# Performance work log

Measured on AMD Instinct MI355X. Metric: run time of the kernel, lower is better.

## Reference

```python
import jax, jax.numpy as jnp
import numpy as np

H, P, G, N, K, CS = 64, 64, 8, 128, 4, 256
HID = 2048
INTER = H * P                      # 4096
CONV_D = INTER + 2 * G * N         # 6144
PROJ = INTER + CONV_D + H          # 10304
EPS = 1e-5


def setup_inputs() -> dict:
    key = jax.random.key(0)
    ks = jax.random.split(key, 4)
    B_, L_ = 2, 2048
    return {
        "hidden_states": jax.random.normal(ks[0], (B_, L_, HID), jnp.float32),
        "in_proj_w": jax.random.normal(ks[1], (PROJ, HID), jnp.float32) * 0.02,
        "conv_w": jax.random.normal(ks[2], (CONV_D, K), jnp.float32) * 0.2,
        "conv_b": jnp.zeros((CONV_D,), jnp.float32),
        "dt_bias": jnp.ones((H,), jnp.float32),
        "A_log": jnp.log(jnp.arange(1, H + 1, dtype=jnp.float32)),
        "D": jnp.ones((H,), jnp.float32),
        "norm_w": jnp.ones((INTER,), jnp.float32),
        "out_proj_w": jax.random.normal(ks[3], (HID, INTER), jnp.float32) * 0.02,
    }


def reference(hidden_states, in_proj_w, conv_w, conv_b, dt_bias, A_log, D, norm_w, out_proj_w):
    b, l, _ = hidden_states.shape
    r = H // G  # heads per group

    zxbcdt = hidden_states @ in_proj_w.T                      # [b,l,PROJ]
    z = zxbcdt[..., :INTER]
    xBC = zxbcdt[..., INTER:INTER + CONV_D]
    dt = zxbcdt[..., INTER + CONV_D:]                          # [b,l,H]

    # causal depthwise conv1d (kernel K, left pad K-1) + SiLU
    xp = jnp.pad(xBC, ((0, 0), (K - 1, 0), (0, 0)))
    conv = conv_b
    for i in range(K):
        conv = conv + conv_w[:, i] * xp[:, i:i + l, :]
    xBC = jax.nn.silu(conv)

    x = xBC[..., :INTER]
    Bm = xBC[..., INTER:INTER + G * N]
    Cm = xBC[..., INTER + G * N:]

    dt = jax.nn.softplus(dt + dt_bias)                         # [b,l,H]
    A = -jnp.exp(A_log)                                        # [H]

    nc = l // CS
    x_c = x.reshape(b, nc, CS, G, r, P)
    dt_c = dt.reshape(b, nc, CS, G, r)
    B_c = Bm.reshape(b, nc, CS, G, N)
    C_c = Cm.reshape(b, nc, CS, G, N)

    dA = dt_c * A.reshape(G, r)                                # [b,nc,c,g,r]
    dA_cs = jnp.cumsum(dA, axis=2)                             # inclusive cumsum over chunk

    # intra-chunk: L[i,j] = exp(dA_cs[i]-dA_cs[j]) for i>=j
    diff = dA_cs[:, :, :, None] - dA_cs[:, :, None]            # [b,nc,i,j,g,r]
    mask = jnp.tril(jnp.ones((CS, CS), bool))[None, None, :, :, None, None]
    Lmat = jnp.exp(jnp.where(mask, diff, -jnp.inf))
    CB = jnp.einsum('bzign,bzjgn->bzijg', C_c, B_c)            # per-group C·B
    M = CB[..., None] * Lmat * dt_c[:, :, None]                # [b,nc,i,j,g,r]
    Y_diag = jnp.einsum('bzijgr,bzjgrp->bzigrp', M, x_c)

    # per-chunk end states
    w = jnp.exp(dA_cs[:, :, -1:] - dA_cs) * dt_c               # decay to chunk end * dt
    states = jnp.einsum('bzjgn,bzjgr,bzjgrp->bzgrpn', B_c, w, x_c)  # [b,nc,g,r,p,n]
    chunk_decay = jnp.exp(dA_cs[:, :, -1])                     # [b,nc,g,r]

    def step(S, inp):
        d, s = inp
        return d[..., None, None] * S + s, S                   # emit state BEFORE chunk

    init = jnp.zeros((b, G, r, P, N), x.dtype)
    _, prev = jax.lax.scan(step, init, (jnp.moveaxis(chunk_decay, 1, 0), jnp.moveaxis(states, 1, 0)))
    prev = jnp.moveaxis(prev, 0, 1)                            # [b,nc,g,r,p,n]

    Y_off = jnp.einsum('bzign,bzgrpn->bzigrp', C_c, prev) * jnp.exp(dA_cs)[..., None]

    Y = (Y_diag + Y_off).reshape(b, l, H, P) + D[:, None] * x.reshape(b, l, H, P)
    y = Y.reshape(b, l, INTER)

    # gated RMSNorm, norm_before_gate=True: out = rmsnorm(y) * silu(z)
    var = jnp.mean(y * y, axis=-1, keepdims=True)
    y = norm_w * (y * jax.lax.rsqrt(var + EPS)) * jax.nn.silu(z)

    return y @ out_proj_w.T
```

## Files before the change

kernel.cpp:

```cpp
#include <hip/hip_runtime.h>
#include <hip/hip_bf16.h>
#include <cstdint>
#include <cstddef>

#define H_     64
#define P_     64
#define G_     8
#define N_     128
#define K_     4
#define CS_    256
#define HID_   2048
#define INTER_ 4096
#define CONVD_ 6144
#define PROJ_  10304
#define ZSTR_  10240
#define B_     2
#define L_     2048
#define NC_    8
#define ML_    4096
#define EPS_   1e-5f

typedef unsigned short ushort_t;
typedef __attribute__((ext_vector_type(8))) short short8;
typedef __attribute__((ext_vector_type(4))) float f32x4;

__device__ inline float b2f(ushort_t v) {
  unsigned u = ((unsigned)v) << 16;
  float f;
  __builtin_memcpy(&f, &u, 4);
  return f;
}
__device__ inline ushort_t f2b(float f) {
  unsigned u;
  __builtin_memcpy(&u, &f, 4);
  u = u + 0x7FFFu + ((u >> 16) & 1u);
  return (ushort_t)(u >> 16);
}
__device__ inline void ld_bf8(const ushort_t* p, float* f) {
  uint4 u = *(const uint4*)p;
  const ushort_t* s = (const ushort_t*)&u;
#pragma unroll
  for (int c = 0; c < 8; ++c) f[c] = b2f(s[c]);
}
__device__ inline void st_bf8(ushort_t* p, const float* f) {
  uint4 u;
  ushort_t* s = (ushort_t*)&u;
#pragma unroll
  for (int c = 0; c < 8; ++c) s[c] = f2b(f[c]);
  *(uint4*)p = u;
}

__global__ __launch_bounds__(256) void cast1_k(const float* __restrict__ hs,
                                               const float* __restrict__ w_in,
                                               ushort_t* __restrict__ hsb,
                                               ushort_t* __restrict__ w_inb) {
  size_t e8 = ((size_t)blockIdx.x * 256 + threadIdx.x) * 8;
  const float* src;
  ushort_t* dst;
  const size_t HSN = (size_t)ML_ * HID_;
  if (e8 < HSN) { src = hs + e8; dst = hsb + e8; }
  else          { src = w_in + (e8 - HSN); dst = w_inb + (e8 - HSN); }
  float4 a = *(const float4*)src;
  float4 b = *(const float4*)(src + 4);
  float v[8] = {a.x, a.y, a.z, a.w, b.x, b.y, b.z, b.w};
  st_bf8(dst, v);
}

typedef const __attribute__((address_space(1))) unsigned int gu32;
typedef __attribute__((address_space(3))) unsigned int lu32;
__device__ __forceinline__ void gl_lds16(const ushort_t* g, ushort_t* l) {
  __builtin_amdgcn_global_load_lds((gu32*)g, (lu32*)l, 16, 0, 0);
}

template<int N> __device__ __forceinline__ void wait_vmcnt() {
  if constexpr (N == 8)      asm volatile("s_waitcnt vmcnt(8)" ::: "memory");
  else if constexpr (N == 6) asm volatile("s_waitcnt vmcnt(6)" ::: "memory");
  else if constexpr (N == 4) asm volatile("s_waitcnt vmcnt(4)" ::: "memory");
  else if constexpr (N == 3) asm volatile("s_waitcnt vmcnt(3)" ::: "memory");
  else                       asm volatile("s_waitcnt vmcnt(0)" ::: "memory");
}

template<int MR>
__device__ __forceinline__ void gemm_core(const ushort_t* __restrict__ Ag,
                                          const ushort_t* __restrict__ Bg,
                                          int lda, int ldb, int nkt,
                                          int bm, int bn, int brmax,
                                          ushort_t* __restrict__ As,
                                          ushort_t* __restrict__ Bs,
                                          f32x4 (&acc)[MR / 32][4]) {
  constexpr int MF = MR / 32;
  constexpr int ASLOT = MR * 32;
  constexpr int BSLOT = 256 * 32;
  constexpr int LPT = (MR == 256) ? 4 : 3;
  const int t = threadIdx.x;
  const int w = t >> 6, l = t & 63;
  const int wm = w >> 2, wn = w & 3;
  const int ml = l & 15, q = l >> 4;
  const int swz = (ml >> 1) & 3;
  const int aoff = (wm * (MR / 2) + ml) * 32 + ((q ^ swz) << 3);
  const int boff = (wn * 64 + ml) * 32 + ((q ^ swz) << 3);
  const int permc = (((l & 3) ^ ((l >> 3) & 3)) << 3);
  const ushort_t* ag0 = Ag + (size_t)(bm + (MR / 8) * w + (l >> 2)) * lda + permc;
  const ushort_t* ag1 = ag0 + (size_t)16 * lda;
  int br0 = bn + 32 * w + (l >> 2);      if (br0 > brmax) br0 = brmax;
  int br1 = bn + 32 * w + 16 + (l >> 2); if (br1 > brmax) br1 = brmax;
  const ushort_t* bg0 = Bg + (size_t)br0 * ldb + permc;
  const ushort_t* bg1 = Bg + (size_t)br1 * ldb + permc;
  ushort_t* alw = As + ((MR == 256) ? (2 * w * 512) : (w * 512));
  ushort_t* blw = Bs + 2 * w * 512;

#define STAGE_A_(kt_)                                                        \
  { const int k_ = (kt_) << 5;                                               \
    ushort_t* sa_ = alw + ((kt_) & 3) * ASLOT;                               \
    gl_lds16(ag0 + k_, sa_);                                                 \
    if (MR == 256) gl_lds16(ag1 + k_, sa_ + 512); }
#define STAGE_B_(kt_)                                                        \
  { const int k_ = (kt_) << 5;                                               \
    ushort_t* sb_ = blw + ((kt_) & 3) * BSLOT;                               \
    gl_lds16(bg0 + k_, sb_);                                                 \
    gl_lds16(bg1 + k_, sb_ + 512); }

  STAGE_A_(0); STAGE_B_(0);
  STAGE_A_(1); STAGE_B_(1);
  STAGE_A_(2); STAGE_B_(2);

#pragma unroll
  for (int i = 0; i < MF; ++i)
#pragma unroll
    for (int j = 0; j < 4; ++j) acc[i][j] = (f32x4){0.f, 0.f, 0.f, 0.f};

#pragma unroll 1
  for (int kt = 0; kt < nkt; ++kt) {
    const ushort_t* Asl = As + (kt & 3) * ASLOT;
    const ushort_t* Bsl = Bs + (kt & 3) * BSLOT;
    if (kt + 2 < nkt)      wait_vmcnt<2 * LPT>();
    else if (kt + 1 < nkt) wait_vmcnt<LPT>();
    else                   wait_vmcnt<0>();
    __builtin_amdgcn_s_barrier();
    asm volatile("" ::: "memory");
    const bool st = (kt + 3) < nkt;
    short8 bfr[4], af[MF / 2];
#pragma unroll
    for (int nf = 0; nf < 4; ++nf)
      bfr[nf] = *(const short8*)(Bsl + boff + nf * 512);
#pragma unroll
    for (int mf = 0; mf < MF / 2; ++mf)
      af[mf] = *(const short8*)(Asl + aoff + mf * 512);
    if (st) STAGE_A_(kt + 3);
    __builtin_amdgcn_s_setprio(1);
#pragma unroll
    for (int mf = 0; mf < MF / 2; ++mf)
#pragma unroll
      for (int nf = 0; nf < 4; ++nf)
        acc[mf][nf] = __builtin_amdgcn_mfma_f32_16x16x32_bf16(af[mf], bfr[nf], acc[mf][nf], 0, 0, 0);
    __builtin_amdgcn_s_setprio(0);
#pragma unroll
    for (int mf = 0; mf < MF / 2; ++mf)
      af[mf] = *(const short8*)(Asl + aoff + (mf + MF / 2) * 512);
    if (st) STAGE_B_(kt + 3);
    __builtin_amdgcn_s_setprio(1);
#pragma unroll
    for (int mf = 0; mf < MF / 2; ++mf)
#pragma unroll
      for (int nf = 0; nf < 4; ++nf)
        acc[mf + MF / 2][nf] = __builtin_amdgcn_mfma_f32_16x16x32_bf16(af[mf], bfr[nf], acc[mf + MF / 2][nf], 0, 0, 0);
    __builtin_amdgcn_s_setprio(0);
  }
#undef STAGE_A_
#undef STAGE_B_
}

__global__ __launch_bounds__(512, 2) void gemm1_256(const ushort_t* __restrict__ hsb,
                                                    const ushort_t* __restrict__ w_inb,
                                                    ushort_t* __restrict__ zb,
                                                    float* __restrict__ dtraw) {
  __shared__ __align__(16) ushort_t As[4 * 8192];
  __shared__ __align__(16) ushort_t Bs[4 * 8192];
  int bid = blockIdx.x;
  int wg = (bid & 7) * 82 + (bid >> 3);
  int tm = wg & 15, tn = wg >> 4;
  int bm = tm * 256, bn = tn * 256;
  f32x4 acc[8][4];
  gemm_core<256>(hsb, w_inb, HID_, HID_, HID_ / 32, bm, bn, PROJ_ - 1, As, Bs, acc);
  int t = threadIdx.x, w = t >> 6, l = t & 63;
  int wm = w >> 2, wn = w & 3, ml = l & 15, quad = l >> 4;
  int rb = bm + wm * 128 + quad * 4;
  int cb = bn + wn * 64 + ml;
  if (tn < 40) {
#pragma unroll
    for (int mf = 0; mf < 8; ++mf)
#pragma unroll
      for (int r = 0; r < 4; ++r) {
        size_t row = (size_t)(rb + mf * 16 + r) * ZSTR_;
#pragma unroll
        for (int nf = 0; nf < 4; ++nf)
          zb[row + cb + nf * 16] = f2b(acc[mf][nf][r]);
      }
  } else if (wn == 0) {
#pragma unroll
    for (int mf = 0; mf < 8; ++mf)
#pragma unroll
      for (int r = 0; r < 4; ++r) {
        int tok = rb + mf * 16 + r;
#pragma unroll
        for (int nf = 0; nf < 4; ++nf)
          dtraw[(size_t)(ml + nf * 16) * ML_ + tok] = acc[mf][nf][r];
      }
  }
}

__global__ __launch_bounds__(512, 2) void gemm2_128(const ushort_t* __restrict__ Ab,
                                                    const ushort_t* __restrict__ Bb,
                                                    float* __restrict__ C) {
  __shared__ __align__(16) ushort_t As[4 * 4096];
  __shared__ __align__(16) ushort_t Bs[4 * 8192];
  int bid = blockIdx.x;
  int wg = (bid & 7) * 32 + (bid >> 3);
  int tm = wg & 31, tn = wg >> 5;
  int bm = tm * 128, bn = tn * 256;
  f32x4 acc[4][4];
  gemm_core<128>(Ab, Bb, CONVD_, INTER_, INTER_ / 32, bm, bn, HID_ - 1, As, Bs, acc);
  int t = threadIdx.x, w = t >> 6, l = t & 63;
  int wm = w >> 2, wn = w & 3, ml = l & 15, quad = l >> 4;
  int rb = bm + wm * 64 + quad * 4;
  int cb = bn + wn * 64 + ml;
#pragma unroll
  for (int mf = 0; mf < 4; ++mf)
#pragma unroll
    for (int r = 0; r < 4; ++r) {
      size_t row = (size_t)(rb + mf * 16 + r) * HID_;
#pragma unroll
      for (int nf = 0; nf < 4; ++nf)
        C[row + cb + nf * 16] = acc[mf][nf][r];
    }
}

#define CROWS_ 8
__global__ __launch_bounds__(256) void conv_dt_k(const ushort_t* __restrict__ zb,
                                                 const float* __restrict__ cw,
                                                 const float* __restrict__ cb,
                                                 ushort_t* __restrict__ xcb,
                                                 const float* __restrict__ dtraw,
                                                 const float* __restrict__ dt_bias,
                                                 const float* __restrict__ A_log,
                                                 float* __restrict__ dtp,
                                                 float* __restrict__ dacs,
                                                 float* __restrict__ cdec) {
  __shared__ float sm[256];
  int bid = blockIdx.x;
  if (bid < 1536) {
    int grp = bid & 511;
    int seg = bid >> 9;
    int u = threadIdx.x;
    int c8 = seg * 2048 + u * 8;
    int row0 = grp * CROWS_;
    int l0 = row0 & (L_ - 1);

    float wv[K_][8], bias[8];
    {
      const float4* wp = (const float4*)(cw + (size_t)c8 * K_);
#pragma unroll
      for (int c = 0; c < 8; ++c) {
        float4 w4 = wp[c];
        wv[0][c] = w4.x; wv[1][c] = w4.y; wv[2][c] = w4.z; wv[3][c] = w4.w;
      }
      float4 b0 = *(const float4*)(cb + c8);
      float4 b1 = *(const float4*)(cb + c8 + 4);
      bias[0] = b0.x; bias[1] = b0.y; bias[2] = b0.z; bias[3] = b0.w;
      bias[4] = b1.x; bias[5] = b1.y; bias[6] = b1.z; bias[7] = b1.w;
    }
    const ushort_t* xin = zb + (size_t)row0 * ZSTR_ + INTER_ + c8;
    ushort_t* xout = xcb + (size_t)row0 * CONVD_ + c8;

    float win[4][8];
#pragma unroll
    for (int i = 0; i < 3; ++i) {
      if (l0 > 0) {
        ld_bf8(xin + (ptrdiff_t)(i - 3) * ZSTR_, win[i]);
      } else {
#pragma unroll
        for (int c = 0; c < 8; ++c) win[i][c] = 0.f;
      }
    }
#pragma unroll
    for (int r = 0; r < CROWS_; ++r) {
      ld_bf8(xin + (size_t)r * ZSTR_, win[(r + 3) & 3]);
      float a[8];
#pragma unroll
      for (int c = 0; c < 8; ++c) {
        float v = bias[c];
        v = fmaf(wv[0][c], win[(r + 0) & 3][c], v);
        v = fmaf(wv[1][c], win[(r + 1) & 3][c], v);
        v = fmaf(wv[2][c], win[(r + 2) & 3][c], v);
        v = fmaf(wv[3][c], win[(r + 3) & 3][c], v);
        a[c] = v / (1.f + __expf(-v));
      }
      st_bf8(xout + (size_t)r * CONVD_, a);
    }
  } else {
    int bzh = bid - 1536;
    int h = bzh & 63, z = (bzh >> 6) & 7, b = bzh >> 9;
    int i = threadIdx.x;
    size_t row = (size_t)b * L_ + z * CS_ + i;
    float dv = dtraw[(size_t)h * ML_ + row] + dt_bias[h];
    float sp = (dv > 20.f) ? dv : log1pf(expf(dv));
    float v = sp * (-expf(A_log[h]));
    sm[i] = v;
    __syncthreads();
    for (int off = 1; off < 256; off <<= 1) {
      float add = (i >= off) ? sm[i - off] : 0.f;
      __syncthreads();
      sm[i] += add;
      __syncthreads();
    }
    float cs = sm[i];
    size_t ob = ((size_t)b * H_ + h) * L_ + z * CS_ + i;
    dtp[ob] = sp;
    dacs[ob] = cs;
    if (i == CS_ - 1) cdec[bzh] = expf(cs);
  }
}

__global__ __launch_bounds__(256) void cb_k(const ushort_t* __restrict__ xcb,
                                            ushort_t* __restrict__ CBo) {
  static const unsigned char itab[10] = {0, 1, 1, 2, 2, 2, 3, 3, 3, 3};
  static const unsigned char jtab[10] = {0, 0, 1, 0, 1, 2, 0, 1, 2, 3};
  int tp = blockIdx.x;
  int it = itab[tp], jt = jtab[tp];
  int bzg = blockIdx.y;
  int g = bzg & 7, z = (bzg >> 3) & 7, b = bzg >> 6;
  int t = threadIdx.x;
  int tx = t & 15, ty = t >> 4;
  __shared__ float CtT[64][68];
  __shared__ float BtT[64][68];
  size_t rowbase = (size_t)b * L_ + (size_t)z * CS_;
  float acc[4][4];
#pragma unroll
  for (int i = 0; i < 4; ++i)
#pragma unroll
    for (int j = 0; j < 4; ++j) acc[i][j] = 0.f;

  for (int half = 0; half < 2; ++half) {
    int nb = half * 64;
    __syncthreads();
#pragma unroll
    for (int u = 0; u < 2; ++u) {
      int idx = t + u * 256;
      int rr = idx >> 3, f = idx & 7;
      float cv[8], bv[8];
      ld_bf8(xcb + (rowbase + it * 64 + rr) * CONVD_ + INTER_ + G_ * N_ + g * N_ + nb + f * 8, cv);
      ld_bf8(xcb + (rowbase + jt * 64 + rr) * CONVD_ + INTER_ + g * N_ + nb + f * 8, bv);
#pragma unroll
      for (int c = 0; c < 8; ++c) { CtT[f * 8 + c][rr] = cv[c]; BtT[f * 8 + c][rr] = bv[c]; }
    }
    __syncthreads();
    for (int n = 0; n < 64; ++n) {
      float4 cv = *(const float4*)&CtT[n][ty * 4];
      float4 bv = *(const float4*)&BtT[n][tx * 4];
      float cc[4] = {cv.x, cv.y, cv.z, cv.w};
      float bb[4] = {bv.x, bv.y, bv.z, bv.w};
#pragma unroll
      for (int i = 0; i < 4; ++i)
#pragma unroll
        for (int j = 0; j < 4; ++j) acc[i][j] = fmaf(cc[i], bb[j], acc[i][j]);
    }
  }
  size_t cbase = ((size_t)((b * 8 + z) * 8 + g)) * (CS_ * CS_);
#pragma unroll
  for (int i = 0; i < 4; ++i) {
    int row = it * 64 + ty * 4 + i;
    ushort4 v;
    v.x = f2b(acc[i][0]); v.y = f2b(acc[i][1]); v.z = f2b(acc[i][2]); v.w = f2b(acc[i][3]);
    *(ushort4*)(CBo + cbase + (size_t)row * CS_ + jt * 64 + tx * 4) = v;
  }
}

__global__ __launch_bounds__(256) void states_mfma(const ushort_t* __restrict__ xcb,
                                                   const float* __restrict__ dacs,
                                                   const float* __restrict__ dtp,
                                                   float* __restrict__ st) {
  int bzh = blockIdx.x;
  int h = bzh & 63, z = (bzh >> 6) & 7, b = bzh >> 9;
  int g = h >> 3;
  int t = threadIdx.x;
  int wv = t >> 6, lane = t & 63;
  int ml = lane & 15, ko = (lane >> 4) * 8;
  __shared__ float ws[256];
  __shared__ __align__(16) ushort_t Xw[64 * 136];
  __shared__ __align__(16) ushort_t Bt[128 * 136];
  size_t base = ((size_t)b * H_ + h) * L_ + z * CS_;
  float dlast = dacs[base + CS_ - 1];
  ws[t] = __expf(dlast - dacs[base + t]) * dtp[base + t];
  size_t rowbase = (size_t)b * L_ + z * CS_;
  f32x4 acc[4][2];
#pragma unroll
  for (int i = 0; i < 4; ++i) {
    acc[i][0] = (f32x4){0.f, 0.f, 0.f, 0.f};
    acc[i][1] = (f32x4){0.f, 0.f, 0.f, 0.f};
  }
  for (int half = 0; half < 2; ++half) {
    int j0 = half * 128;
    __syncthreads();
    {
      int jl = t >> 1, pseg = (t & 1) * 32;
      const ushort_t* xr = xcb + (rowbase + j0 + jl) * CONVD_ + h * P_ + pseg;
      float wj = ws[j0 + jl];
#pragma unroll
      for (int q = 0; q < 4; ++q) {
        float v[8];
        ld_bf8(xr + q * 8, v);
#pragma unroll
        for (int c = 0; c < 8; ++c) Xw[(pseg + q * 8 + c) * 136 + jl] = f2b(v[c] * wj);
      }
    }
    {
      int jl = t >> 1, nseg = (t & 1) * 64;
      const ushort_t* br = xcb + (rowbase + j0 + jl) * CONVD_ + INTER_ + g * N_ + nseg;
#pragma unroll
      for (int q = 0; q < 8; ++q) {
        uint4 raw = *(const uint4*)(br + q * 8);
        const ushort_t* s = (const ushort_t*)&raw;
#pragma unroll
        for (int c = 0; c < 8; ++c) Bt[(nseg + q * 8 + c) * 136 + jl] = s[c];
      }
    }
    __syncthreads();
#pragma unroll
    for (int k0 = 0; k0 < 128; k0 += 32) {
      short8 af[4], bf2[2];
#pragma unroll
      for (int mf = 0; mf < 4; ++mf)
        af[mf] = *(const short8*)(Xw + (mf * 16 + ml) * 136 + k0 + ko);
#pragma unroll
      for (int nf = 0; nf < 2; ++nf)
        bf2[nf] = *(const short8*)(Bt + (wv * 32 + nf * 16 + ml) * 136 + k0 + ko);
#pragma unroll
      for (int mf = 0; mf < 4; ++mf)
#pragma unroll
        for (int nf = 0; nf < 2; ++nf)
          acc[mf][nf] = __builtin_amdgcn_mfma_f32_16x16x32_bf16(af[mf], bf2[nf], acc[mf][nf], 0, 0, 0);
    }
  }
  float* outp = st + ((size_t)((b * 8 + z) * H_ + h)) * (P_ * N_);
  int quad = lane >> 4;
#pragma unroll
  for (int mf = 0; mf < 4; ++mf)
#pragma unroll
    for (int nf = 0; nf < 2; ++nf) {
      int n = wv * 32 + nf * 16 + ml;
#pragma unroll
      for (int r = 0; r < 4; ++r) {
        int p = mf * 16 + quad * 4 + r;
        outp[(size_t)p * N_ + n] = acc[mf][nf][r];
      }
    }
}

__global__ __launch_bounds__(256) void scan_k(float* __restrict__ st,
                                              const float* __restrict__ cdec) {
  size_t idx = (size_t)blockIdx.x * 256 + threadIdx.x;
  int b = (int)(idx >> 19);
  size_t rem = idx & 524287;
  int h = (int)(rem >> 13);
  float S = 0.f;
#pragma unroll
  for (int z = 0; z < NC_; ++z) {
    size_t off = (size_t)(b * 8 + z) * 524288 + rem;
    float old = st[off];
    st[off] = S;
    S = cdec[(b * 8 + z) * H_ + h] * S + old;
  }
}

__global__ __launch_bounds__(256) void y_mfma(const ushort_t* xcb,
                                              const ushort_t* __restrict__ CB,
                                              const float* __restrict__ pv,
                                              const float* __restrict__ dacs,
                                              const float* __restrict__ dtp,
                                              const float* __restrict__ Dw,
                                              ushort_t* Yx) {
  int bzh = blockIdx.x;
  int h = bzh & 63, z = (bzh >> 6) & 7, b = bzh >> 9;
  int g = h >> 3;
  int t = threadIdx.x;
  int wv = t >> 6, lane = t & 63;
  int ml = lane & 15, quad = lane >> 4, ko = quad * 8;
  __shared__ __align__(16) ushort_t Ms[256 * 40];
  __shared__ __align__(16) ushort_t XsYs[18432];
  __shared__ __align__(16) ushort_t Ps[64 * 136];
  __shared__ float dAs[256], dts[256];

  size_t rowbase = (size_t)b * L_ + z * CS_;
  {
    size_t base = ((size_t)b * H_ + h) * L_ + z * CS_;
    dAs[t] = dacs[base + t];
    dts[t] = dtp[base + t];
  }
  {
    int p = t >> 2, c0 = (t & 3) * 32;
    const float* pr = pv + ((size_t)((b * 8 + z) * H_ + h)) * (P_ * N_) + (size_t)p * N_ + c0;
    ushort_t* dst = Ps + p * 136 + c0;
#pragma unroll
    for (int u = 0; u < 4; ++u) {
      float4 a = *(const float4*)(pr + u * 8);
      float4 bq = *(const float4*)(pr + u * 8 + 4);
      float v[8] = {a.x, a.y, a.z, a.w, bq.x, bq.y, bq.z, bq.w};
      st_bf8(dst + u * 8, v);
    }
  }
  {
    const ushort_t* xr = xcb + (rowbase + t) * CONVD_ + h * P_;
    ushort_t* Xs = XsYs;
#pragma unroll
    for (int q = 0; q < 8; ++q) {
      uint4 raw = *(const uint4*)(xr + q * 8);
      const ushort_t* s = (const ushort_t*)&raw;
#pragma unroll
      for (int c = 0; c < 8; ++c) Xs[(q * 8 + c) * 264 + t] = s[c];
    }
  }

  f32x4 acc[4][4];
#pragma unroll
  for (int i = 0; i < 4; ++i)
#pragma unroll
    for (int j = 0; j < 4; ++j) acc[i][j] = (f32x4){0.f, 0.f, 0.f, 0.f};

  int cOff = INTER_ + G_ * N_ + g * N_;
#pragma unroll
  for (int k0 = 0; k0 < 128; k0 += 32) {
    __syncthreads();
#pragma unroll
    for (int u = 0; u < 4; ++u) {
      int sid = u * 256 + t;
      int row = sid >> 2, kc = (sid & 3) * 8;
      gl_lds16(xcb + (rowbase + row) * CONVD_ + cOff + k0 + kc,
               Ms + (size_t)(u * 256 + wv * 64) * 8);
    }
    __syncthreads();
    short8 af[4], bf[4];
#pragma unroll
    for (int mf = 0; mf < 4; ++mf)
      af[mf] = *(const short8*)(Ps + (mf * 16 + ml) * 136 + k0 + ko);
#pragma unroll
    for (int nf = 0; nf < 4; ++nf)
      bf[nf] = *(const short8*)(Ms + (wv * 64 + nf * 16 + ml) * 32 + ko);
#pragma unroll
    for (int mf = 0; mf < 4; ++mf)
#pragma unroll
      for (int nf = 0; nf < 4; ++nf)
        acc[mf][nf] = __builtin_amdgcn_mfma_f32_16x16x32_bf16(af[mf], bf[nf], acc[mf][nf], 0, 0, 0);
  }
#pragma unroll
  for (int nf = 0; nf < 4; ++nf) {
    float e = __expf(dAs[wv * 64 + nf * 16 + ml]);
#pragma unroll
    for (int mf = 0; mf < 4; ++mf) {
      acc[mf][nf][0] *= e; acc[mf][nf][1] *= e;
      acc[mf][nf][2] *= e; acc[mf][nf][3] *= e;
    }
  }

  float dAi_t = dAs[t];
  size_t cbase = ((size_t)((b * 8 + z) * 8 + g)) * (CS_ * CS_) + (size_t)t * CS_;
  const ushort_t* Xs = XsYs;
  for (int j0 = 0; j0 < 256; j0 += 32) {
    __syncthreads();
    {
      const ushort_t* cbr = CB + cbase + j0;
      ushort_t* mrow = Ms + t * 40;
#pragma unroll
      for (int q = 0; q < 4; ++q) {
        float cv[8], o[8];
        ld_bf8(cbr + q * 8, cv);
#pragma unroll
        for (int c = 0; c < 8; ++c) {
          int j = j0 + q * 8 + c;
          float m = cv[c] * __expf(dAi_t - dAs[j]) * dts[j];
          o[c] = (j <= t) ? m : 0.f;
        }
        st_bf8(mrow + q * 8, o);
      }
    }
    __syncthreads();
    short8 af[4], bf[4];
#pragma unroll
    for (int mf = 0; mf < 4; ++mf)
      af[mf] = *(const short8*)(Xs + (mf * 16 + ml) * 264 + j0 + ko);
#pragma unroll
    for (int nf = 0; nf < 4; ++nf)
      bf[nf] = *(const short8*)(Ms + (wv * 64 + nf * 16 + ml) * 40 + ko);
#pragma unroll
    for (int mf = 0; mf < 4; ++mf)
#pragma unroll
      for (int nf = 0; nf < 4; ++nf)
        acc[mf][nf] = __builtin_amdgcn_mfma_f32_16x16x32_bf16(af[mf], bf[nf], acc[mf][nf], 0, 0, 0);
  }

  __syncthreads();
  ushort_t* Ys = XsYs;
#pragma unroll
  for (int mf = 0; mf < 4; ++mf)
#pragma unroll
    for (int nf = 0; nf < 4; ++nf) {
      int iw = wv * 64 + nf * 16 + ml;
      int pb = mf * 16 + quad * 4;
      uint2 pk;
      ushort_t* s = (ushort_t*)&pk;
      s[0] = f2b(acc[mf][nf][0]); s[1] = f2b(acc[mf][nf][1]);
      s[2] = f2b(acc[mf][nf][2]); s[3] = f2b(acc[mf][nf][3]);
      *(uint2*)(Ys + iw * 72 + pb) = pk;
    }
  __syncthreads();
  {
    float Dh = Dw[h];
    const ushort_t* xr = xcb + (rowbase + t) * CONVD_ + h * P_;
    ushort_t* yr = Yx + (rowbase + t) * CONVD_ + h * P_;
#pragma unroll
    for (int q = 0; q < 8; ++q) {
      float xv[8], yv[8], o[8];
      ld_bf8(xr + q * 8, xv);
      ld_bf8(Ys + t * 72 + q * 8, yv);
#pragma unroll
      for (int c = 0; c < 8; ++c) o[c] = yv[c] + Dh * xv[c];
      st_bf8(yr + q * 8, o);
    }
  }
}

__global__ __launch_bounds__(256) void rms_cast2_k(ushort_t* __restrict__ Y,
                                                   const ushort_t* __restrict__ zb,
                                                   const float* __restrict__ nw,
                                                   const float* __restrict__ w_out,
                                                   ushort_t* __restrict__ w_outb) {
  __shared__ float red[4];
  int bid = blockIdx.x;
  int t = threadIdx.x;
  if (bid >= ML_) {
    size_t e8 = ((size_t)(bid - ML_) * 256 + t) * 8;
    float4 a = *(const float4*)(w_out + e8);
    float4 b = *(const float4*)(w_out + e8 + 4);
    float v[8] = {a.x, a.y, a.z, a.w, b.x, b.y, b.z, b.w};
    st_bf8(w_outb + e8, v);
    return;
  }
  int row = bid;
  ushort_t* y = Y + (size_t)row * CONVD_;
  const ushort_t* zp = zb + (size_t)row * ZSTR_;
  float v[2][8];
  float s = 0.f;
#pragma unroll
  for (int u = 0; u < 2; ++u) {
    ld_bf8(y + u * 2048 + t * 8, v[u]);
#pragma unroll
    for (int c = 0; c < 8; ++c) s += v[u][c] * v[u][c];
  }
#pragma unroll
  for (int off = 32; off > 0; off >>= 1) s += __shfl_down(s, off);
  if ((t & 63) == 0) red[t >> 6] = s;
  __syncthreads();
  float tot = red[0] + red[1] + red[2] + red[3];
  float rstd = rsqrtf(tot * (1.f / INTER_) + EPS_);
#pragma unroll
  for (int u = 0; u < 2; ++u) {
    int c0 = u * 2048 + t * 8;
    float zv[8], o[8];
    ld_bf8(zp + c0, zv);
    float4 w0 = *(const float4*)(nw + c0);
    float4 w1 = *(const float4*)(nw + c0 + 4);
    float wv[8] = {w0.x, w0.y, w0.z, w0.w, w1.x, w1.y, w1.z, w1.w};
#pragma unroll
    for (int c = 0; c < 8; ++c)
      o[c] = wv[c] * v[u][c] * rstd * (zv[c] / (1.f + __expf(-zv[c])));
    st_bf8(y + c0, o);
  }
}

extern "C" void kernel_launch(void* const* d_in, const int* in_sizes, int n_in,
                              void* d_out, int out_size, void* d_ws, size_t ws_size,
                              hipStream_t stream) {
  const float* hs    = (const float*)d_in[0];
  const float* w_in  = (const float*)d_in[1];
  const float* cw    = (const float*)d_in[2];
  const float* cb    = (const float*)d_in[3];
  const float* dtb   = (const float*)d_in[4];
  const float* alog  = (const float*)d_in[5];
  const float* Dw    = (const float*)d_in[6];
  const float* nw    = (const float*)d_in[7];
  const float* w_out = (const float*)d_in[8];
  float* out = (float*)d_out;

  char* base = (char*)d_ws;
  ushort_t* zb    = (ushort_t*)(base);
  ushort_t* xcb   = (ushort_t*)(base + 83886080);
  float*    dtraw = (float*)(base + 134217728);
  float*    dtp   = (float*)(base + 135266304);
  float*    dacs  = (float*)(base + 136314880);
  float*    cdec  = (float*)(base + 137363456);
  char*     R1    = base + 137367552;
  char*     R2    = base + 154144768;
  ushort_t* hsb    = (ushort_t*)R1;
  ushort_t* cbuf   = (ushort_t*)R1;
  ushort_t* w_outb = (ushort_t*)R1;
  ushort_t* w_inb  = (ushort_t*)R2;
  float*    st     = (float*)R2;

  cast1_k<<<14400, 256, 0, stream>>>(hs, w_in, hsb, w_inb);
  gemm1_256<<<656, 512, 0, stream>>>(hsb, w_inb, zb, dtraw);
  conv_dt_k<<<2560, 256, 0, stream>>>(zb, cw, cb, xcb, dtraw, dtb, alog, dtp, dacs, cdec);
  cb_k<<<dim3(10, B_ * NC_ * G_), 256, 0, stream>>>(xcb, cbuf);
  states_mfma<<<B_ * NC_ * H_, 256, 0, stream>>>(xcb, dacs, dtp, st);
  scan_k<<<(B_ * H_ * P_ * N_) / 256, 256, 0, stream>>>(st, cdec);
  y_mfma<<<B_ * NC_ * H_, 256, 0, stream>>>(xcb, cbuf, st, dacs, dtp, Dw, xcb);
  rms_cast2_k<<<8192, 256, 0, stream>>>(xcb, zb, nw, w_out, w_outb);
  gemm2_128<<<256, 512, 0, stream>>>(xcb, w_outb, out);
}
```

Measured before the change: 629.6 us.

## Use MFMA for C·B chunk products, pack LDS transposes, prefetch CB tiles

The cb_k kernel now stages C and B tiles into LDS as bf16 with direct global-to-LDS loads and an XOR swizzle. It then computes the 64x64 block with bf16 MFMA instructions in place of scalar fp32 FMAs. In states_mfma, the transposed X and B tiles are written as packed 32-bit pairs of adjacent rows, which halves the number of LDS stores. In the diagonal output kernel, the next 32-column slice of the CB matrix is register-prefetched during the MFMA loop to hide global load latency. The final per-element scalar bf16 stores in cb_k may be less coalesced than the previous 4-wide stores.

```diff
diff --git a/kernel.cpp b/kernel.cpp
--- a/kernel.cpp
+++ b/kernel.cpp
@@ -330,49 +330,63 @@
   int bzg = blockIdx.y;
   int g = bzg & 7, z = (bzg >> 3) & 7, b = bzg >> 6;
   int t = threadIdx.x;
-  int tx = t & 15, ty = t >> 4;
-  __shared__ float CtT[64][68];
-  __shared__ float BtT[64][68];
+  int w = t >> 6, l = t & 63;
+  __shared__ __align__(16) ushort_t Cs[64 * 128];
+  __shared__ __align__(16) ushort_t Bs[64 * 128];
   size_t rowbase = (size_t)b * L_ + (size_t)z * CS_;
-  float acc[4][4];
-#pragma unroll
-  for (int i = 0; i < 4; ++i)
-#pragma unroll
-    for (int j = 0; j < 4; ++j) acc[i][j] = 0.f;
-
-  for (int half = 0; half < 2; ++half) {
-    int nb = half * 64;
-    __syncthreads();
-#pragma unroll
-    for (int u = 0; u < 2; ++u) {
-      int idx = t + u * 256;
-      int rr = idx >> 3, f = idx & 7;
-      float cv[8], bv[8];
-      ld_bf8(xcb + (rowbase + it * 64 + rr) * CONVD_ + INTER_ + G_ * N_ + g * N_ + nb + f * 8, cv);
-      ld_bf8(xcb + (rowbase + jt * 64 + rr) * CONVD_ + INTER_ + g * N_ + nb + f * 8, bv);
-#pragma unroll
-      for (int c = 0; c < 8; ++c) { CtT[f * 8 + c][rr] = cv[c]; BtT[f * 8 + c][rr] = bv[c]; }
-    }
-    __syncthreads();
-    for (int n = 0; n < 64; ++n) {
-      float4 cv = *(const float4*)&CtT[n][ty * 4];
-      float4 bv = *(const float4*)&BtT[n][tx * 4];
-      float cc[4] = {cv.x, cv.y, cv.z, cv.w};
-      float bb[4] = {bv.x, bv.y, bv.z, bv.w};
-#pragma unroll
-      for (int i = 0; i < 4; ++i)
-#pragma unroll
-        for (int j = 0; j < 4; ++j) acc[i][j] = fmaf(cc[i], bb[j], acc[i][j]);
-    }
+  {
+    int s = l & 15;
+    int cO = INTER_ + G_ * N_ + g * N_;
+    int bO = INTER_ + g * N_;
+#pragma unroll
+    for (int i = 0; i < 4; ++i) {
+      int row = 16 * w + 4 * i + (l >> 4);
+      int src = ((s ^ (row & 15)) << 3);
+      gl_lds16(xcb + (rowbase + it * 64 + row) * CONVD_ + cO + src,
+               Cs + (16 * w + 4 * i) * 128);
+      gl_lds16(xcb + (rowbase + jt * 64 + row) * CONVD_ + bO + src,
+               Bs + (16 * w + 4 * i) * 128);
+    }
+  }
+  asm volatile("s_waitcnt vmcnt(0)" ::: "memory");
+  __builtin_amdgcn_s_barrier();
+  int wm = w >> 1, wn = w & 1;
+  int ml = l & 15, q = l >> 4;
+  f32x4 acc[2][2];
+#pragma unroll
+  for (int i = 0; i < 2; ++i)
+#pragma unroll
+    for (int j = 0; j < 2; ++j) acc[i][j] = (f32x4){0.f, 0.f, 0.f, 0.f};
+#pragma unroll
+  for (int kk = 0; kk < 4; ++kk) {
+    short8 af[2], bf[2];
+#pragma unroll
+    for (int mf = 0; mf < 2; ++mf) {
+      int row = wm * 32 + mf * 16 + ml;
+      af[mf] = *(const short8*)(Cs + row * 128 + (((kk * 4 + q) ^ (row & 15)) << 3));
+    }
+#pragma unroll
+    for (int nf = 0; nf < 2; ++nf) {
+      int row = wn * 32 + nf * 16 + ml;
+      bf[nf] = *(const short8*)(Bs + row * 128 + (((kk * 4 + q) ^ (row & 15)) << 3));
+    }
+#pragma unroll
+    for (int mf = 0; mf < 2; ++mf)
+#pragma unroll
+      for (int nf = 0; nf < 2; ++nf)
+        acc[mf][nf] = __builtin_amdgcn_mfma_f32_16x16x32_bf16(af[mf], bf[nf], acc[mf][nf], 0, 0, 0);
   }
   size_t cbase = ((size_t)((b * 8 + z) * 8 + g)) * (CS_ * CS_);
 #pragma unroll
-  for (int i = 0; i < 4; ++i) {
-    int row = it * 64 + ty * 4 + i;
-    ushort4 v;
-    v.x = f2b(acc[i][0]); v.y = f2b(acc[i][1]); v.z = f2b(acc[i][2]); v.w = f2b(acc[i][3]);
-    *(ushort4*)(CBo + cbase + (size_t)row * CS_ + jt * 64 + tx * 4) = v;
-  }
+  for (int mf = 0; mf < 2; ++mf)
+#pragma unroll
+    for (int nf = 0; nf < 2; ++nf)
+#pragma unroll
+      for (int r = 0; r < 4; ++r) {
+        int i = wm * 32 + mf * 16 + q * 4 + r;
+        int j = wn * 32 + nf * 16 + ml;
+        CBo[cbase + (size_t)(it * 64 + i) * CS_ + jt * 64 + j] = f2b(acc[mf][nf][r]);
+      }
 }
 
 __global__ __launch_bounds__(256) void states_mfma(const ushort_t* __restrict__ xcb,
@@ -402,26 +416,41 @@
     int j0 = half * 128;
     __syncthreads();
     {
-      int jl = t >> 1, pseg = (t & 1) * 32;
-      const ushort_t* xr = xcb + (rowbase + j0 + jl) * CONVD_ + h * P_ + pseg;
-      float wj = ws[j0 + jl];
-#pragma unroll
-      for (int q = 0; q < 4; ++q) {
-        float v[8];
-        ld_bf8(xr + q * 8, v);
-#pragma unroll
-        for (int c = 0; c < 8; ++c) Xw[(pseg + q * 8 + c) * 136 + jl] = f2b(v[c] * wj);
+      int j2 = (t & 63) * 2, pseg = (t >> 6) * 16;
+      const ushort_t* xr0 = xcb + (rowbase + j0 + j2) * CONVD_ + h * P_ + pseg;
+      const ushort_t* xr1 = xr0 + CONVD_;
+      float w0 = ws[j0 + j2], w1 = ws[j0 + j2 + 1];
+      float v0[8], v0b[8], v1[8], v1b[8];
+      ld_bf8(xr0, v0); ld_bf8(xr0 + 8, v0b);
+      ld_bf8(xr1, v1); ld_bf8(xr1 + 8, v1b);
+      unsigned* xw32 = (unsigned*)Xw;
+      int col = t & 63;
+#pragma unroll
+      for (int pp = 0; pp < 8; ++pp) {
+        unsigned lo = f2b(v0[pp] * w0), hi = f2b(v1[pp] * w1);
+        xw32[(pseg + pp) * 68 + col] = lo | (hi << 16);
+      }
+#pragma unroll
+      for (int pp = 0; pp < 8; ++pp) {
+        unsigned lo = f2b(v0b[pp] * w0), hi = f2b(v1b[pp] * w1);
+        xw32[(pseg + 8 + pp) * 68 + col] = lo | (hi << 16);
       }
     }
     {
-      int jl = t >> 1, nseg = (t & 1) * 64;
-      const ushort_t* br = xcb + (rowbase + j0 + jl) * CONVD_ + INTER_ + g * N_ + nseg;
-#pragma unroll
-      for (int q = 0; q < 8; ++q) {
-        uint4 raw = *(const uint4*)(br + q * 8);
-        const ushort_t* s = (const ushort_t*)&raw;
-#pragma unroll
-        for (int c = 0; c < 8; ++c) Bt[(nseg + q * 8 + c) * 136 + jl] = s[c];
+      int j2 = (t & 63) * 2, nseg = (t >> 6) * 32;
+      const ushort_t* br0 = xcb + (rowbase + j0 + j2) * CONVD_ + INTER_ + g * N_ + nseg;
+      const ushort_t* br1 = br0 + CONVD_;
+      unsigned* bt32 = (unsigned*)Bt;
+      int col = t & 63;
+#pragma unroll
+      for (int qq = 0; qq < 4; ++qq) {
+        uint4 r0 = *(const uint4*)(br0 + qq * 8);
+        uint4 r1 = *(const uint4*)(br1 + qq * 8);
+        const ushort_t* s0 = (const ushort_t*)&r0;
+        const ushort_t* s1 = (const ushort_t*)&r1;
+#pragma unroll
+        for (int c = 0; c < 8; ++c)
+          bt32[(nseg + qq * 8 + c) * 68 + col] = (unsigned)s0[c] | ((unsigned)s1[c] << 16);
       }
     }
     __syncthreads();
@@ -564,23 +593,34 @@
   float dAi_t = dAs[t];
   size_t cbase = ((size_t)((b * 8 + z) * 8 + g)) * (CS_ * CS_) + (size_t)t * CS_;
   const ushort_t* Xs = XsYs;
+  uint4 pre[4];
+  {
+    const ushort_t* cbr = CB + cbase;
+#pragma unroll
+    for (int qq = 0; qq < 4; ++qq) pre[qq] = *(const uint4*)(cbr + qq * 8);
+  }
   for (int j0 = 0; j0 < 256; j0 += 32) {
     __syncthreads();
     {
-      const ushort_t* cbr = CB + cbase + j0;
       ushort_t* mrow = Ms + t * 40;
 #pragma unroll
-      for (int q = 0; q < 4; ++q) {
-        float cv[8], o[8];
-        ld_bf8(cbr + q * 8, cv);
+      for (int qq = 0; qq < 4; ++qq) {
+        const ushort_t* s = (const ushort_t*)&pre[qq];
+        float o[8];
 #pragma unroll
         for (int c = 0; c < 8; ++c) {
-          int j = j0 + q * 8 + c;
-          float m = cv[c] * __expf(dAi_t - dAs[j]) * dts[j];
+          int j = j0 + qq * 8 + c;
+          float m = b2f(s[c]) * __expf(dAi_t - dAs[j]) * dts[j];
           o[c] = (j <= t) ? m : 0.f;
         }
-        st_bf8(mrow + q * 8, o);
-      }
+        st_bf8(mrow + qq * 8, o);
+      }
+    }
+    uint4 nxt[4];
+    if (j0 + 32 < 256) {
+      const ushort_t* cbr = CB + cbase + j0 + 32;
+#pragma unroll
+      for (int qq = 0; qq < 4; ++qq) nxt[qq] = *(const uint4*)(cbr + qq * 8);
     }
     __syncthreads();
     short8 af[4], bf[4];
@@ -595,6 +635,8 @@
 #pragma unroll
       for (int nf = 0; nf < 4; ++nf)
         acc[mf][nf] = __builtin_amdgcn_mfma_f32_16x16x32_bf16(af[mf], bf[nf], acc[mf][nf], 0, 0, 0);
+#pragma unroll
+    for (int qq = 0; qq < 4; ++qq) pre[qq] = nxt[qq];
   }
 
   __syncthreads();
```

New measurement: 627.3 us. Within noise of the previous version (-0.4%).
